# Optimization experiments

Hardware: AMD Instinct MI355X
Metric: run time of the kernel (lower is better)

The kernel has to match this reference:

```python
import jax, jax.numpy as jnp
import numpy as np

B, D, F, H = 256, 9, 8, 256   # batch of trees, tree depth, input features, hidden
N = 2 ** (D + 1) - 1          # total nodes per full binary tree (heap layout)


def _init(key, shape, fan_in):
    return jax.random.normal(key, shape, jnp.float32) * (1.0 / np.sqrt(fan_in))


def setup_inputs() -> dict:
    key = jax.random.key(0)
    ks = jax.random.split(key, 6)
    return {
        "data": jax.random.normal(ks[0], (B, N, F), jnp.float32),
        "Wu": _init(ks[1], (H, F), F),
        "bu": jnp.zeros((H,), jnp.float32),
        "Wr": _init(ks[2], (3 * H, 3 * H), 3 * H),
        "br": jnp.zeros((3 * H,), jnp.float32),
        "Wh": _init(ks[3], (H, 3 * H), 3 * H),
        "bh": jnp.zeros((H,), jnp.float32),
        "Wz": _init(ks[4], (4 * H, 4 * H), 4 * H),
        "bz": jnp.zeros((4 * H,), jnp.float32),
        "Wp": _init(ks[5], (1, H), H),
        "bp": jnp.zeros((1,), jnp.float32),
    }


def reference(data, Wu, bu, Wr, br, Wh, bh, Wz, bz, Wp, bp):
    # data: [B, N, F] node features in heap (level-order) layout;
    # children of the i-th node of level l are nodes 2i, 2i+1 of level l+1.
    b, n_nodes, _ = data.shape
    L = (n_nodes + 1) // 2          # number of leaves
    depth = L.bit_length() - 1
    h_dim = Wu.shape[0]

    # leaf embedding u for every node (leaf() is applied at every tree node)
    u = jnp.einsum('bnf,hf->bnh', data, Wu) + bu          # [B, N, H]
    h = u[:, L - 1:, :]                                    # leaf level states [B, L, H]

    for l in range(depth - 1, -1, -1):                     # bottom-up over levels
        n = 2 ** l
        parent = u[:, n - 1:2 * n - 1, :]                  # [B, n, H]
        h_l, h_r = h[:, 0::2, :], h[:, 1::2, :]            # [B, n, H] each
        hhu = jnp.concatenate([parent, h_l, h_r], axis=-1)  # [B, n, 3H]
        r = jax.nn.sigmoid(jnp.einsum('bnk,jk->bnj', hhu, Wr) + br)
        h_new = jax.nn.relu(jnp.einsum('bnk,hk->bnh', r * hhu, Wh) + bh)
        hhhu = jnp.concatenate([h_new, hhu], axis=-1)      # [B, n, 4H]
        zlin = jnp.einsum('bnk,jk->bnj', hhhu, Wz) + bz    # [B, n, 4H]
        z = jax.nn.softmax(zlin.reshape(b, n, 4, h_dim), axis=2)
        h = (z * hhhu.reshape(b, n, 4, h_dim)).sum(axis=2)  # gated combine -> [B, n, H]

    # h is [B, 1, H] at the root; logits head
    logits = jnp.einsum('bnh,oh->bno', h, Wp) + bp          # [B, 1, 1]
    return logits[:, 0, 0]                                  # [B]
```

## Files before the change

### kernel.cpp

```cpp
#include <hip/hip_runtime.h>
#include <math.h>

#define BB 256
#define NN 1023
#define FF 8
#define HH 256
#define DEPTH 9

enum { EPI_NONE = 0, EPI_SIGMUL = 1, EPI_RELU = 2, EPI_COMBINE = 3 };

typedef __bf16 bf16x8_t __attribute__((ext_vector_type(8)));
typedef float f32x4_t __attribute__((ext_vector_type(4)));

__device__ __forceinline__ void stage16(const void* g, void* l) {
    __builtin_amdgcn_global_load_lds(
        (const __attribute__((address_space(1))) void*)g,
        (__attribute__((address_space(3))) void*)l,
        16, 0, 0);
}

template <int EPI>
__global__ __launch_bounds__(512, 2) void gemm256p(
    const __bf16* __restrict__ A, int lda,
    const __bf16* __restrict__ W,
    const float* __restrict__ bias,
    const __bf16* __restrict__ aux, int ldaux,
    void* __restrict__ Cout, int ldc,
    int K)
{
    __shared__ __bf16 lds[2][2][256 * 64];
    const int tid = threadIdx.x;
    const int lane = tid & 63;
    const int w = tid >> 6;
    const int wr = w >> 2, wc = w & 3;

    const int nwg = gridDim.x * gridDim.y;
    const int hw = blockIdx.y * gridDim.x + blockIdx.x;
    const int xcd = hw & 7, k0 = hw >> 3;
    const int qq = nwg >> 3, rr = nwg & 7;
    const int wg = (xcd < rr ? xcd * (qq + 1) : rr * (qq + 1) + (xcd - rr) * qq) + k0;
    const int bm0 = (wg / gridDim.x) * 256;
    const int bn0 = (wg % gridDim.x) * 256;

    const int srow = tid >> 3;
    const int scolz = ((tid & 7) ^ ((tid >> 3) & 7)) * 8;

    f32x4_t acc[8][4];
#pragma unroll
    for (int i = 0; i < 8; ++i)
#pragma unroll
        for (int j = 0; j < 4; ++j) acc[i][j] = (f32x4_t){0.f, 0.f, 0.f, 0.f};

    const int rA = lane & 15;
    const int klane = (lane >> 4) * 8;
    const int rxor = (lane & 7) * 8;
    const int NT = K >> 6;

#define STAGE_T(t, buf)                                                        \
    do {                                                                       \
        const int kk_ = (t) << 6;                                              \
        _Pragma("unroll")                                                      \
        for (int rnd = 0; rnd < 4; ++rnd) {                                    \
            stage16(A + (size_t)(bm0 + rnd * 64 + srow) * lda + kk_ + scolz,   \
                    &lds[buf][0][rnd * 4096 + w * 512]);                       \
            stage16(W + (size_t)(bn0 + rnd * 64 + srow) * K + kk_ + scolz,     \
                    &lds[buf][1][rnd * 4096 + w * 512]);                       \
        }                                                                      \
    } while (0)

#define LDA_F(As_, i, ks) \
    (*(const bf16x8_t*)&(As_)[(wr * 128 + (i) * 16 + rA) * 64 + (((ks) * 32 + klane) ^ rxor)])
#define LDB_F(Bs_, j, ks) \
    (*(const bf16x8_t*)&(Bs_)[(wc * 64 + (j) * 16 + rA) * 64 + (((ks) * 32 + klane) ^ rxor)])

    STAGE_T(0, 0);
    STAGE_T(1, 1);
    asm volatile("s_waitcnt vmcnt(8)" ::: "memory");
    __builtin_amdgcn_sched_barrier(0);
    __builtin_amdgcn_s_barrier();
    __builtin_amdgcn_sched_barrier(0);

    for (int t = 0; t < NT; ++t) {
        const int p = t & 1;
        const __bf16* As = lds[p][0];
        const __bf16* Bs = lds[p][1];

        bf16x8_t b0[4], b1[4], alo[4], ahi[4];
#pragma unroll
        for (int j = 0; j < 4; ++j) b0[j] = LDB_F(Bs, j, 0);
#pragma unroll
        for (int i = 0; i < 4; ++i) alo[i] = LDA_F(As, i, 0);
#pragma unroll
        for (int i = 0; i < 4; ++i)
#pragma unroll
            for (int j = 0; j < 4; ++j)
                acc[i][j] = __builtin_amdgcn_mfma_f32_16x16x32_bf16(
                    alo[i], b0[j], acc[i][j], 0, 0, 0);
#pragma unroll
        for (int i = 0; i < 4; ++i) ahi[i] = LDA_F(As, 4 + i, 0);
#pragma unroll
        for (int i = 0; i < 4; ++i)
#pragma unroll
            for (int j = 0; j < 4; ++j)
                acc[4 + i][j] = __builtin_amdgcn_mfma_f32_16x16x32_bf16(
                    ahi[i], b0[j], acc[4 + i][j], 0, 0, 0);
#pragma unroll
        for (int j = 0; j < 4; ++j) b1[j] = LDB_F(Bs, j, 1);
#pragma unroll
        for (int i = 0; i < 4; ++i) alo[i] = LDA_F(As, i, 1);
#pragma unroll
        for (int i = 0; i < 4; ++i) ahi[i] = LDA_F(As, 4 + i, 1);
#pragma unroll
        for (int i = 0; i < 4; ++i)
#pragma unroll
            for (int j = 0; j < 4; ++j)
                acc[i][j] = __builtin_amdgcn_mfma_f32_16x16x32_bf16(
                    alo[i], b1[j], acc[i][j], 0, 0, 0);

        asm volatile("s_waitcnt lgkmcnt(0)" ::: "memory");
        __builtin_amdgcn_sched_barrier(0);
        __builtin_amdgcn_s_barrier();
        __builtin_amdgcn_sched_barrier(0);

        if (t + 2 < NT) STAGE_T(t + 2, p);

        __builtin_amdgcn_s_setprio(1);
#pragma unroll
        for (int i = 0; i < 4; ++i)
#pragma unroll
            for (int j = 0; j < 4; ++j)
                acc[4 + i][j] = __builtin_amdgcn_mfma_f32_16x16x32_bf16(
                    ahi[i], b1[j], acc[4 + i][j], 0, 0, 0);
        __builtin_amdgcn_s_setprio(0);

        if (t + 1 < NT) {
            if (t + 2 < NT) {
                asm volatile("s_waitcnt vmcnt(8)" ::: "memory");
            } else {
                asm volatile("s_waitcnt vmcnt(0)" ::: "memory");
            }
            __builtin_amdgcn_sched_barrier(0);
            __builtin_amdgcn_s_barrier();
            __builtin_amdgcn_sched_barrier(0);
        }
    }
#undef STAGE_T
#undef LDA_F
#undef LDB_F

    if (EPI == EPI_COMBINE) {
        const int r = lane & 15;
        const int G = ((bn0 + wc * 64) >> 2) + r;
        float bz4[4];
#pragma unroll
        for (int g = 0; g < 4; ++g) bz4[g] = bias[bn0 + wc * 64 + g * 16 + r];
#pragma unroll
        for (int i = 0; i < 8; ++i) {
#pragma unroll
            for (int reg = 0; reg < 4; ++reg) {
                const int gr = bm0 + wr * 128 + i * 16 + (lane >> 4) * 4 + reg;
                float z0 = acc[i][0][reg] + bz4[0];
                float z1 = acc[i][1][reg] + bz4[1];
                float z2 = acc[i][2][reg] + bz4[2];
                float z3 = acc[i][3][reg] + bz4[3];
                float mx = fmaxf(fmaxf(z0, z1), fmaxf(z2, z3));
                float e0 = __expf(z0 - mx), e1 = __expf(z1 - mx);
                float e2 = __expf(z2 - mx), e3 = __expf(z3 - mx);
                const __bf16* hrow = aux + (size_t)gr * ldaux + G;
                float hv = (e0 * (float)hrow[0] + e1 * (float)hrow[256] +
                            e2 * (float)hrow[512] + e3 * (float)hrow[768]) /
                           (e0 + e1 + e2 + e3);
                ((__bf16*)Cout)[(size_t)gr * ldc + G] = (__bf16)hv;
            }
        }
    } else {
#pragma unroll
        for (int j = 0; j < 4; ++j) {
            const int gc = bn0 + wc * 64 + j * 16 + (lane & 15);
            const float bv = bias[gc];
#pragma unroll
            for (int i = 0; i < 8; ++i) {
#pragma unroll
                for (int reg = 0; reg < 4; ++reg) {
                    const int gr = bm0 + wr * 128 + i * 16 + (lane >> 4) * 4 + reg;
                    float v = acc[i][j][reg] + bv;
                    if (EPI == EPI_SIGMUL) {
                        float s = 1.0f / (1.0f + __expf(-v));
                        v = s * (float)aux[(size_t)gr * ldaux + gc];
                        ((__bf16*)Cout)[(size_t)gr * ldc + gc] = (__bf16)v;
                    } else if (EPI == EPI_RELU) {
                        v = fmaxf(v, 0.0f);
                        ((__bf16*)Cout)[(size_t)gr * ldc + gc] = (__bf16)v;
                    } else {
                        ((float*)Cout)[(size_t)gr * ldc + gc] = v;
                    }
                }
            }
        }
    }
}

template <int EPI>
__global__ __launch_bounds__(256) void gemm_mfma(
    const __bf16* __restrict__ A, int lda,
    const __bf16* __restrict__ W,
    const float* __restrict__ bias,
    const __bf16* __restrict__ aux, int ldaux,
    void* __restrict__ Cout, int ldc,
    int K)
{
    __shared__ __bf16 As[128 * 32];
    __shared__ __bf16 Bs[128 * 32];
    const int tid = threadIdx.x;
    const int lane = tid & 63;
    const int w = tid >> 6;
    const int wr = w >> 1, wc = w & 1;

    const int nwg = gridDim.x * gridDim.y;
    const int hw = blockIdx.y * gridDim.x + blockIdx.x;
    const int xcd = hw & 7, k0 = hw >> 3;
    const int qq = nwg >> 3, rr = nwg & 7;
    const int wg = (xcd < rr ? xcd * (qq + 1) : rr * (qq + 1) + (xcd - rr) * qq) + k0;
    const int bm0 = (wg / gridDim.x) * 128;
    const int bn0 = (wg % gridDim.x) * 128;

    const int srow = lane >> 2;
    const int scol = (lane & 3) * 8;

    f32x4_t acc[4][4];
#pragma unroll
    for (int i = 0; i < 4; ++i)
#pragma unroll
        for (int j = 0; j < 4; ++j) acc[i][j] = (f32x4_t){0.f, 0.f, 0.f, 0.f};

    const int rA = lane & 15;
    const int kslot = (lane >> 4) * 8;

    for (int kk = 0; kk < K; kk += 32) {
        stage16(A + (size_t)(bm0 + w * 16 + srow) * lda + kk + scol,
                &As[(w * 16) * 32]);
        stage16(A + (size_t)(bm0 + 64 + w * 16 + srow) * lda + kk + scol,
                &As[(64 + w * 16) * 32]);
        stage16(W + (size_t)(bn0 + w * 16 + srow) * K + kk + scol,
                &Bs[(w * 16) * 32]);
        stage16(W + (size_t)(bn0 + 64 + w * 16 + srow) * K + kk + scol,
                &Bs[(64 + w * 16) * 32]);
        __syncthreads();

        bf16x8_t af[4], bfr[4];
#pragma unroll
        for (int i = 0; i < 4; ++i)
            af[i] = *(const bf16x8_t*)&As[(wr * 64 + i * 16 + rA) * 32 + kslot];
#pragma unroll
        for (int j = 0; j < 4; ++j)
            bfr[j] = *(const bf16x8_t*)&Bs[(wc * 64 + j * 16 + rA) * 32 + kslot];
#pragma unroll
        for (int i = 0; i < 4; ++i)
#pragma unroll
            for (int j = 0; j < 4; ++j)
                acc[i][j] = __builtin_amdgcn_mfma_f32_16x16x32_bf16(
                    af[i], bfr[j], acc[i][j], 0, 0, 0);
        __syncthreads();
    }

    if (EPI == EPI_COMBINE) {
        const int r = lane & 15;
        const int G = ((bn0 + wc * 64) >> 2) + r;
        float bz4[4];
#pragma unroll
        for (int g = 0; g < 4; ++g) bz4[g] = bias[bn0 + wc * 64 + g * 16 + r];
#pragma unroll
        for (int i = 0; i < 4; ++i) {
#pragma unroll
            for (int reg = 0; reg < 4; ++reg) {
                const int gr = bm0 + wr * 64 + i * 16 + (lane >> 4) * 4 + reg;
                float z0 = acc[i][0][reg] + bz4[0];
                float z1 = acc[i][1][reg] + bz4[1];
                float z2 = acc[i][2][reg] + bz4[2];
                float z3 = acc[i][3][reg] + bz4[3];
                float mx = fmaxf(fmaxf(z0, z1), fmaxf(z2, z3));
                float e0 = __expf(z0 - mx), e1 = __expf(z1 - mx);
                float e2 = __expf(z2 - mx), e3 = __expf(z3 - mx);
                const __bf16* hrow = aux + (size_t)gr * ldaux + G;
                float hv = (e0 * (float)hrow[0] + e1 * (float)hrow[256] +
                            e2 * (float)hrow[512] + e3 * (float)hrow[768]) /
                           (e0 + e1 + e2 + e3);
                ((__bf16*)Cout)[(size_t)gr * ldc + G] = (__bf16)hv;
            }
        }
    } else {
#pragma unroll
        for (int j = 0; j < 4; ++j) {
            const int gc = bn0 + wc * 64 + j * 16 + (lane & 15);
            const float bv = bias[gc];
#pragma unroll
            for (int i = 0; i < 4; ++i) {
#pragma unroll
                for (int reg = 0; reg < 4; ++reg) {
                    const int gr = bm0 + wr * 64 + i * 16 + (lane >> 4) * 4 + reg;
                    float v = acc[i][j][reg] + bv;
                    if (EPI == EPI_SIGMUL) {
                        float s = 1.0f / (1.0f + __expf(-v));
                        v = s * (float)aux[(size_t)gr * ldaux + gc];
                        ((__bf16*)Cout)[(size_t)gr * ldc + gc] = (__bf16)v;
                    } else if (EPI == EPI_RELU) {
                        v = fmaxf(v, 0.0f);
                        ((__bf16*)Cout)[(size_t)gr * ldc + gc] = (__bf16)v;
                    } else {
                        ((float*)Cout)[(size_t)gr * ldc + gc] = v;
                    }
                }
            }
        }
    }
}

__global__ __launch_bounds__(256) void convert_weights(
    const float* __restrict__ Wr, const float* __restrict__ Wh,
    const float* __restrict__ Wz, const float* __restrict__ bz,
    __bf16* __restrict__ Wrb, __bf16* __restrict__ Whb,
    __bf16* __restrict__ Wzb, float* __restrict__ bzp)
{
    const int NR = 768 * 768, NH2 = 256 * 768, NZ = 1024 * 1024;
    const int idx0 = blockIdx.x * 256 + threadIdx.x;
    for (int i = idx0; i < NR + NH2 + NZ; i += gridDim.x * 256) {
        if (i < NR) Wrb[i] = (__bf16)Wr[i];
        else if (i < NR + NH2) Whb[i - NR] = (__bf16)Wh[i - NR];
        else {
            const int z = i - NR - NH2;
            const int p = z >> 10, k = z & 1023;
            const int o = ((p >> 4) & 3) * 256 + (p >> 6) * 16 + (p & 15);
            Wzb[z] = (__bf16)Wz[(size_t)o * 1024 + k];
        }
    }
    if (idx0 < 1024) {
        const int p = idx0;
        const int o = ((p >> 4) & 3) * 256 + (p >> 6) * 16 + (p & 15);
        bzp[p] = bz[o];
    }
}

__global__ __launch_bounds__(256) void build_hhu(
    const float* __restrict__ data, const float* __restrict__ Wu,
    const float* __restrict__ bu, const __bf16* __restrict__ hprev,
    __bf16* __restrict__ hhhu, int l, int r0)
{
    const int n = 1 << l;
    const int row = blockIdx.x * 8 + (threadIdx.x >> 5);
    const int c0 = (threadIdx.x & 31) * 8;
    const int i = r0 + row;
    const int b = i >> l;
    const int m = i & (n - 1);

    float wv[8][8];
#pragma unroll
    for (int cc = 0; cc < 8; ++cc) {
        float4 w0 = *(const float4*)&Wu[(c0 + cc) * 8];
        float4 w1 = *(const float4*)&Wu[(c0 + cc) * 8 + 4];
        wv[cc][0] = w0.x; wv[cc][1] = w0.y; wv[cc][2] = w0.z; wv[cc][3] = w0.w;
        wv[cc][4] = w1.x; wv[cc][5] = w1.y; wv[cc][6] = w1.z; wv[cc][7] = w1.w;
    }
    float buv[8];
#pragma unroll
    for (int cc = 0; cc < 8; ++cc) buv[cc] = bu[c0 + cc];

    __bf16* rowp = hhhu + (size_t)row * 1024;

    {
        const float* dp = data + ((size_t)b * NN + (n - 1) + m) * FF;
        float4 d0 = *(const float4*)dp, d1 = *(const float4*)(dp + 4);
        float dv[8] = {d0.x, d0.y, d0.z, d0.w, d1.x, d1.y, d1.z, d1.w};
        bf16x8_t o;
#pragma unroll
        for (int cc = 0; cc < 8; ++cc) {
            float acc = buv[cc];
#pragma unroll
            for (int f = 0; f < 8; ++f) acc += dv[f] * wv[cc][f];
            o[cc] = (__bf16)acc;
        }
        *(bf16x8_t*)&rowp[256 + c0] = o;
    }

    if (l == 8) {
        const float* dl = data + ((size_t)b * NN + 511 + 2 * m) * FF;
#pragma unroll
        for (int side = 0; side < 2; ++side) {
            const float* dp = dl + side * FF;
            float4 d0 = *(const float4*)dp, d1 = *(const float4*)(dp + 4);
            float dv[8] = {d0.x, d0.y, d0.z, d0.w, d1.x, d1.y, d1.z, d1.w};
            bf16x8_t o;
#pragma unroll
            for (int cc = 0; cc < 8; ++cc) {
                float acc = buv[cc];
#pragma unroll
                for (int f = 0; f < 8; ++f) acc += dv[f] * wv[cc][f];
                o[cc] = (__bf16)acc;
            }
            *(bf16x8_t*)&rowp[512 + side * 256 + c0] = o;
        }
    } else {
        *(bf16x8_t*)&rowp[512 + c0] =
            *(const bf16x8_t*)&hprev[((size_t)b * (2 * n) + 2 * m) * HH + c0];
        *(bf16x8_t*)&rowp[768 + c0] =
            *(const bf16x8_t*)&hprev[((size_t)b * (2 * n) + 2 * m + 1) * HH + c0];
    }
}

__global__ __launch_bounds__(256) void final_kernel(
    const __bf16* __restrict__ hfin, const float* __restrict__ Wp,
    const float* __restrict__ bp, float* __restrict__ out)
{
    const int b = blockIdx.x;
    const int t = threadIdx.x;
    __shared__ float red[256];
    red[t] = (float)hfin[(size_t)b * HH + t] * Wp[t];
    __syncthreads();
    for (int s = 128; s > 0; s >>= 1) {
        if (t < s) red[t] += red[t + s];
        __syncthreads();
    }
    if (t == 0) out[b] = red[0] + bp[0];
}

extern "C" void kernel_launch(void* const* d_in, const int* in_sizes, int n_in,
                              void* d_out, int out_size, void* d_ws, size_t ws_size,
                              hipStream_t stream)
{
    const float* data = (const float*)d_in[0];
    const float* Wu = (const float*)d_in[1];
    const float* bu = (const float*)d_in[2];
    const float* Wr = (const float*)d_in[3];
    const float* br = (const float*)d_in[4];
    const float* Wh = (const float*)d_in[5];
    const float* bh = (const float*)d_in[6];
    const float* Wz = (const float*)d_in[7];
    const float* bz = (const float*)d_in[8];
    const float* Wp = (const float*)d_in[9];
    const float* bp = (const float*)d_in[10];
    float* out = (float*)d_out;

    const size_t CAP = 32768;
    char* w = (char*)d_ws;
    __bf16* hA = (__bf16*)w;   w += (size_t)65536 * HH * 2;
    __bf16* hB = (__bf16*)w;   w += (size_t)32768 * HH * 2;
    __bf16* hhhu = (__bf16*)w; w += CAP * 1024 * 2;
    __bf16* rh = (__bf16*)w;   w += CAP * 768 * 2;
    __bf16* Wrb = (__bf16*)w;  w += (size_t)768 * 768 * 2;
    __bf16* Whb = (__bf16*)w;  w += (size_t)256 * 768 * 2;
    __bf16* Wzb = (__bf16*)w;  w += (size_t)1024 * 1024 * 2;
    float* bzp = (float*)w;    w += 1024 * 4;

    convert_weights<<<2048, 256, 0, stream>>>(Wr, Wh, Wz, bz, Wrb, Whb, Wzb, bzp);

    for (int l = DEPTH - 1; l >= 0; --l) {
        const size_t M = (size_t)BB << l;
        __bf16* dst = ((DEPTH - 1 - l) & 1) ? hB : hA;
        const __bf16* src = ((DEPTH - 1 - l) & 1) ? hA : hB;
        for (size_t r0 = 0; r0 < M; r0 += CAP) {
            const int R = (int)((M - r0 < CAP) ? (M - r0) : CAP);
            build_hhu<<<R / 8, 256, 0, stream>>>(data, Wu, bu, src, hhhu, l, (int)r0);
            if (R >= 2048) {
                gemm256p<EPI_SIGMUL><<<dim3(3, R / 256), 512, 0, stream>>>(
                    hhhu + 256, 1024, Wrb, br, hhhu + 256, 1024, rh, 768, 768);
            } else {
                gemm_mfma<EPI_SIGMUL><<<dim3(6, R / 128), 256, 0, stream>>>(
                    hhhu + 256, 1024, Wrb, br, hhhu + 256, 1024, rh, 768, 768);
            }
            gemm_mfma<EPI_RELU><<<dim3(2, R / 128), 256, 0, stream>>>(
                rh, 768, Whb, bh, nullptr, 0, hhhu, 1024, 768);
            if (R >= 2048) {
                gemm256p<EPI_COMBINE><<<dim3(4, R / 256), 512, 0, stream>>>(
                    hhhu, 1024, Wzb, bzp, hhhu, 1024,
                    dst + (size_t)r0 * HH, HH, 1024);
            } else {
                gemm_mfma<EPI_COMBINE><<<dim3(8, R / 128), 256, 0, stream>>>(
                    hhhu, 1024, Wzb, bzp, hhhu, 1024,
                    dst + (size_t)r0 * HH, HH, 1024);
            }
        }
    }
    final_kernel<<<BB, 256, 0, stream>>>(hA, Wp, bp, out);
}
```

Baseline: 1.240 ms.

## Split GEMM main loop into four phases with interleaved quarter-tile prefetch

The 256x256 bf16 GEMM main loop is reorganised into four barrier-delimited MFMA phases per K-tile. Each phase issues one quarter of the next tile's global-to-LDS loads, A row-quarters and B column-halves, instead of staging whole tiles two iterations ahead. Finer vmcnt waits let a phase start once the part of the tile it needs has landed, and setprio is raised around each MFMA block. Launch bounds drop to one workgroup per CU, trading occupancy for register headroom, and the extra barriers could add synchronisation cost.

```diff
diff --git a/kernel.cpp b/kernel.cpp
--- a/kernel.cpp
+++ b/kernel.cpp
@@ -20,7 +20,7 @@
 }
 
 template <int EPI>
-__global__ __launch_bounds__(512, 2) void gemm256p(
+__global__ __launch_bounds__(512, 1) void gemm256p(
     const __bf16* __restrict__ A, int lda,
     const __bf16* __restrict__ W,
     const float* __restrict__ bias,
@@ -43,7 +43,7 @@
     const int bn0 = (wg % gridDim.x) * 256;
 
     const int srow = tid >> 3;
-    const int scolz = ((tid & 7) ^ ((tid >> 3) & 7)) * 8;
+    const int scolz = ((tid & 7) ^ (srow & 7)) * 8;
 
     f32x4_t acc[8][4];
 #pragma unroll
@@ -56,16 +56,21 @@
     const int rxor = (lane & 7) * 8;
     const int NT = K >> 6;
 
-#define STAGE_T(t, buf)                                                        \
+#define STAGE_A_Q(t, buf, q)                                                   \
     do {                                                                       \
         const int kk_ = (t) << 6;                                              \
-        _Pragma("unroll")                                                      \
-        for (int rnd = 0; rnd < 4; ++rnd) {                                    \
-            stage16(A + (size_t)(bm0 + rnd * 64 + srow) * lda + kk_ + scolz,   \
-                    &lds[buf][0][rnd * 4096 + w * 512]);                       \
-            stage16(W + (size_t)(bn0 + rnd * 64 + srow) * K + kk_ + scolz,     \
-                    &lds[buf][1][rnd * 4096 + w * 512]);                       \
-        }                                                                      \
+        stage16(A + (size_t)(bm0 + (q) * 64 + srow) * lda + kk_ + scolz,       \
+                &lds[buf][0][((q) * 64) * 64 + w * 512]);                      \
+        stage16(A + (size_t)(bm0 + 128 + (q) * 64 + srow) * lda + kk_ + scolz, \
+                &lds[buf][0][((128 + (q) * 64)) * 64 + w * 512]);              \
+    } while (0)
+#define STAGE_B_H(t, buf, hf)                                                  \
+    do {                                                                       \
+        const int kk_ = (t) << 6;                                              \
+        stage16(W + (size_t)(bn0 + (hf) * 128 + srow) * K + kk_ + scolz,       \
+                &lds[buf][1][((hf) * 128) * 64 + w * 512]);                    \
+        stage16(W + (size_t)(bn0 + (hf) * 128 + 64 + srow) * K + kk_ + scolz,  \
+                &lds[buf][1][((hf) * 128 + 64) * 64 + w * 512]);               \
     } while (0)
 
 #define LDA_F(As_, i, ks) \
@@ -73,80 +78,106 @@
 #define LDB_F(Bs_, j, ks) \
     (*(const bf16x8_t*)&(Bs_)[(wc * 64 + (j) * 16 + rA) * 64 + (((ks) * 32 + klane) ^ rxor)])
 
-    STAGE_T(0, 0);
-    STAGE_T(1, 1);
-    asm volatile("s_waitcnt vmcnt(8)" ::: "memory");
+#define PHASE_OPEN()                         \
+    __builtin_amdgcn_sched_barrier(0);       \
+    __builtin_amdgcn_s_barrier();            \
+    asm volatile("s_waitcnt lgkmcnt(0)" ::: "memory"); \
+    __builtin_amdgcn_sched_barrier(0);       \
+    __builtin_amdgcn_s_setprio(1)
+#define PHASE_CLOSE()                        \
+    __builtin_amdgcn_s_setprio(0);           \
+    __builtin_amdgcn_sched_barrier(0);       \
+    __builtin_amdgcn_s_barrier();            \
+    __builtin_amdgcn_sched_barrier(0)
+
+    STAGE_A_Q(0, 0, 0);
+    STAGE_A_Q(0, 0, 1);
+    STAGE_B_H(0, 0, 0);
+    STAGE_B_H(0, 0, 1);
+    asm volatile("s_waitcnt vmcnt(0)" ::: "memory");
     __builtin_amdgcn_sched_barrier(0);
     __builtin_amdgcn_s_barrier();
     __builtin_amdgcn_sched_barrier(0);
 
     for (int t = 0; t < NT; ++t) {
-        const int p = t & 1;
-        const __bf16* As = lds[p][0];
-        const __bf16* Bs = lds[p][1];
-
-        bf16x8_t b0[4], b1[4], alo[4], ahi[4];
+        const int c = t & 1, n = c ^ 1;
+        const __bf16* As = lds[c][0];
+        const __bf16* Bs = lds[c][1];
+        const bool more = (t + 1 < NT);
+        bf16x8_t a0[4], a1[4], b0[4], b1[4];
+
 #pragma unroll
         for (int j = 0; j < 4; ++j) b0[j] = LDB_F(Bs, j, 0);
 #pragma unroll
-        for (int i = 0; i < 4; ++i) alo[i] = LDA_F(As, i, 0);
+        for (int i = 0; i < 4; ++i) a0[i] = LDA_F(As, i, 0);
+        if (more) STAGE_A_Q(t + 1, n, 0);
+        PHASE_OPEN();
 #pragma unroll
         for (int i = 0; i < 4; ++i)
 #pragma unroll
             for (int j = 0; j < 4; ++j)
                 acc[i][j] = __builtin_amdgcn_mfma_f32_16x16x32_bf16(
-                    alo[i], b0[j], acc[i][j], 0, 0, 0);
-#pragma unroll
-        for (int i = 0; i < 4; ++i) ahi[i] = LDA_F(As, 4 + i, 0);
-#pragma unroll
-        for (int i = 0; i < 4; ++i)
-#pragma unroll
-            for (int j = 0; j < 4; ++j)
-                acc[4 + i][j] = __builtin_amdgcn_mfma_f32_16x16x32_bf16(
-                    ahi[i], b0[j], acc[4 + i][j], 0, 0, 0);
+                    a0[i], b0[j], acc[i][j], 0, 0, 0);
+        PHASE_CLOSE();
+
 #pragma unroll
         for (int j = 0; j < 4; ++j) b1[j] = LDB_F(Bs, j, 1);
 #pragma unroll
-        for (int i = 0; i < 4; ++i) alo[i] = LDA_F(As, i, 1);
-#pragma unroll
-        for (int i = 0; i < 4; ++i) ahi[i] = LDA_F(As, 4 + i, 1);
+        for (int i = 0; i < 4; ++i) a1[i] = LDA_F(As, i, 1);
+        if (more) STAGE_B_H(t + 1, n, 0);
+        PHASE_OPEN();
 #pragma unroll
         for (int i = 0; i < 4; ++i)
 #pragma unroll
             for (int j = 0; j < 4; ++j)
                 acc[i][j] = __builtin_amdgcn_mfma_f32_16x16x32_bf16(
-                    alo[i], b1[j], acc[i][j], 0, 0, 0);
-
-        asm volatile("s_waitcnt lgkmcnt(0)" ::: "memory");
+                    a1[i], b1[j], acc[i][j], 0, 0, 0);
+        __builtin_amdgcn_s_setprio(0);
+        if (more) {
+            asm volatile("s_waitcnt vmcnt(4)" ::: "memory");
+        } else {
+            asm volatile("s_waitcnt vmcnt(0)" ::: "memory");
+        }
         __builtin_amdgcn_sched_barrier(0);
         __builtin_amdgcn_s_barrier();
         __builtin_amdgcn_sched_barrier(0);
 
-        if (t + 2 < NT) STAGE_T(t + 2, p);
-
-        __builtin_amdgcn_s_setprio(1);
+#pragma unroll
+        for (int i = 0; i < 4; ++i) a0[i] = LDA_F(As, 4 + i, 0);
+        if (more) STAGE_B_H(t + 1, n, 1);
+        PHASE_OPEN();
 #pragma unroll
         for (int i = 0; i < 4; ++i)
 #pragma unroll
             for (int j = 0; j < 4; ++j)
                 acc[4 + i][j] = __builtin_amdgcn_mfma_f32_16x16x32_bf16(
-                    ahi[i], b1[j], acc[4 + i][j], 0, 0, 0);
+                    a0[i], b0[j], acc[4 + i][j], 0, 0, 0);
+        PHASE_CLOSE();
+
+#pragma unroll
+        for (int i = 0; i < 4; ++i) a1[i] = LDA_F(As, 4 + i, 1);
+        if (more) STAGE_A_Q(t + 1, n, 1);
+        PHASE_OPEN();
+#pragma unroll
+        for (int i = 0; i < 4; ++i)
+#pragma unroll
+            for (int j = 0; j < 4; ++j)
+                acc[4 + i][j] = __builtin_amdgcn_mfma_f32_16x16x32_bf16(
+                    a1[i], b1[j], acc[4 + i][j], 0, 0, 0);
         __builtin_amdgcn_s_setprio(0);
-
-        if (t + 1 < NT) {
-            if (t + 2 < NT) {
-                asm volatile("s_waitcnt vmcnt(8)" ::: "memory");
-            } else {
-                asm volatile("s_waitcnt vmcnt(0)" ::: "memory");
-            }
-            __builtin_amdgcn_sched_barrier(0);
-            __builtin_amdgcn_s_barrier();
-            __builtin_amdgcn_sched_barrier(0);
-        }
-    }
-#undef STAGE_T
+        if (more) {
+            asm volatile("s_waitcnt vmcnt(2)" ::: "memory");
+        }
+        __builtin_amdgcn_sched_barrier(0);
+        __builtin_amdgcn_s_barrier();
+        __builtin_amdgcn_sched_barrier(0);
+    }
+#undef STAGE_A_Q
+#undef STAGE_B_H
 #undef LDA_F
 #undef LDB_F
+#undef PHASE_OPEN
+#undef PHASE_CLOSE
 
     if (EPI == EPI_COMBINE) {
         const int r = lane & 15;
```

After: 1.259 ms. No clear change (+1.5%).

## Use 16-wave workgroups in 256x256 GEMM and XCD-remap build_hhu blocks

Applied to the files above, without the earlier changes.

The 256x256-tile GEMM now launches 1024 threads (16 waves in a 4x4 layout), so each wave owns a 64x64 output subtile instead of 128x64. This halves per-wave accumulators and fragment registers, and each thread stages four 16-byte chunks per k-step instead of eight. The aim is more waves in flight to hide LDS and global latency. It also drops the sched_barrier fences, which gives the compiler more freedom but weakens control of the interleaving. build_hhu block indices are remapped per XCD for locality.

```diff
diff --git a/kernel.cpp b/kernel.cpp
--- a/kernel.cpp
+++ b/kernel.cpp
@@ -19,8 +19,14 @@
         16, 0, 0);
 }
 
+__device__ __forceinline__ int xcd_remap(int hw, int nwg) {
+    const int xcd = hw & 7, k0 = hw >> 3;
+    const int qq = nwg >> 3, rr = nwg & 7;
+    return (xcd < rr ? xcd * (qq + 1) : rr * (qq + 1) + (xcd - rr) * qq) + k0;
+}
+
 template <int EPI>
-__global__ __launch_bounds__(512, 2) void gemm256p(
+__global__ __launch_bounds__(1024, 4) void gemm256w(
     const __bf16* __restrict__ A, int lda,
     const __bf16* __restrict__ W,
     const float* __restrict__ bias,
@@ -36,18 +42,16 @@
 
     const int nwg = gridDim.x * gridDim.y;
     const int hw = blockIdx.y * gridDim.x + blockIdx.x;
-    const int xcd = hw & 7, k0 = hw >> 3;
-    const int qq = nwg >> 3, rr = nwg & 7;
-    const int wg = (xcd < rr ? xcd * (qq + 1) : rr * (qq + 1) + (xcd - rr) * qq) + k0;
+    const int wg = xcd_remap(hw, nwg);
     const int bm0 = (wg / gridDim.x) * 256;
     const int bn0 = (wg % gridDim.x) * 256;
 
     const int srow = tid >> 3;
-    const int scolz = ((tid & 7) ^ ((tid >> 3) & 7)) * 8;
-
-    f32x4_t acc[8][4];
-#pragma unroll
-    for (int i = 0; i < 8; ++i)
+    const int scolz = ((tid & 7) ^ (srow & 7)) * 8;
+
+    f32x4_t acc[4][4];
+#pragma unroll
+    for (int i = 0; i < 4; ++i)
 #pragma unroll
         for (int j = 0; j < 4; ++j) acc[i][j] = (f32x4_t){0.f, 0.f, 0.f, 0.f};
 
@@ -59,106 +63,91 @@
 #define STAGE_T(t, buf)                                                        \
     do {                                                                       \
         const int kk_ = (t) << 6;                                              \
-        _Pragma("unroll")                                                      \
-        for (int rnd = 0; rnd < 4; ++rnd) {                                    \
-            stage16(A + (size_t)(bm0 + rnd * 64 + srow) * lda + kk_ + scolz,   \
-                    &lds[buf][0][rnd * 4096 + w * 512]);                       \
-            stage16(W + (size_t)(bn0 + rnd * 64 + srow) * K + kk_ + scolz,     \
-                    &lds[buf][1][rnd * 4096 + w * 512]);                       \
-        }                                                                      \
+        stage16(A + (size_t)(bm0 + srow) * lda + kk_ + scolz,                  \
+                &lds[buf][0][w * 512]);                                        \
+        stage16(A + (size_t)(bm0 + 128 + srow) * lda + kk_ + scolz,            \
+                &lds[buf][0][8192 + w * 512]);                                 \
+        stage16(W + (size_t)(bn0 + srow) * K + kk_ + scolz,                    \
+                &lds[buf][1][w * 512]);                                        \
+        stage16(W + (size_t)(bn0 + 128 + srow) * K + kk_ + scolz,              \
+                &lds[buf][1][8192 + w * 512]);                                 \
     } while (0)
-
 #define LDA_F(As_, i, ks) \
-    (*(const bf16x8_t*)&(As_)[(wr * 128 + (i) * 16 + rA) * 64 + (((ks) * 32 + klane) ^ rxor)])
+    (*(const bf16x8_t*)&(As_)[(wr * 64 + (i) * 16 + rA) * 64 + (((ks) * 32 + klane) ^ rxor)])
 #define LDB_F(Bs_, j, ks) \
     (*(const bf16x8_t*)&(Bs_)[(wc * 64 + (j) * 16 + rA) * 64 + (((ks) * 32 + klane) ^ rxor)])
 
     STAGE_T(0, 0);
     STAGE_T(1, 1);
-    asm volatile("s_waitcnt vmcnt(8)" ::: "memory");
-    __builtin_amdgcn_sched_barrier(0);
+    asm volatile("s_waitcnt vmcnt(4)" ::: "memory");
     __builtin_amdgcn_s_barrier();
-    __builtin_amdgcn_sched_barrier(0);
 
     for (int t = 0; t < NT; ++t) {
-        const int p = t & 1;
-        const __bf16* As = lds[p][0];
-        const __bf16* Bs = lds[p][1];
-
-        bf16x8_t b0[4], b1[4], alo[4], ahi[4];
-#pragma unroll
-        for (int j = 0; j < 4; ++j) b0[j] = LDB_F(Bs, j, 0);
-#pragma unroll
-        for (int i = 0; i < 4; ++i) alo[i] = LDA_F(As, i, 0);
+        const int cur = t & 1;
+        const __bf16* As = lds[cur][0];
+        const __bf16* Bs = lds[cur][1];
+        bf16x8_t af[4], bf[4];
+
+#pragma unroll
+        for (int j = 0; j < 4; ++j) bf[j] = LDB_F(Bs, j, 0);
+#pragma unroll
+        for (int i = 0; i < 4; ++i) af[i] = LDA_F(As, i, 0);
 #pragma unroll
         for (int i = 0; i < 4; ++i)
 #pragma unroll
             for (int j = 0; j < 4; ++j)
                 acc[i][j] = __builtin_amdgcn_mfma_f32_16x16x32_bf16(
-                    alo[i], b0[j], acc[i][j], 0, 0, 0);
-#pragma unroll
-        for (int i = 0; i < 4; ++i) ahi[i] = LDA_F(As, 4 + i, 0);
-#pragma unroll
-        for (int i = 0; i < 4; ++i)
-#pragma unroll
-            for (int j = 0; j < 4; ++j)
-                acc[4 + i][j] = __builtin_amdgcn_mfma_f32_16x16x32_bf16(
-                    ahi[i], b0[j], acc[4 + i][j], 0, 0, 0);
-#pragma unroll
-        for (int j = 0; j < 4; ++j) b1[j] = LDB_F(Bs, j, 1);
-#pragma unroll
-        for (int i = 0; i < 4; ++i) alo[i] = LDA_F(As, i, 1);
-#pragma unroll
-        for (int i = 0; i < 4; ++i) ahi[i] = LDA_F(As, 4 + i, 1);
-#pragma unroll
-        for (int i = 0; i < 4; ++i)
+                    af[i], bf[j], acc[i][j], 0, 0, 0);
+#pragma unroll
+        for (int j = 0; j < 4; ++j) bf[j] = LDB_F(Bs, j, 1);
+#pragma unroll
+        for (int i = 0; i < 4; ++i) af[i] = LDA_F(As, i, 1);
+#pragma unroll
+        for (int i = 0; i < 2; ++i)
 #pragma unroll
             for (int j = 0; j < 4; ++j)
                 acc[i][j] = __builtin_amdgcn_mfma_f32_16x16x32_bf16(
-                    alo[i], b1[j], acc[i][j], 0, 0, 0);
+                    af[i], bf[j], acc[i][j], 0, 0, 0);
 
         asm volatile("s_waitcnt lgkmcnt(0)" ::: "memory");
-        __builtin_amdgcn_sched_barrier(0);
         __builtin_amdgcn_s_barrier();
-        __builtin_amdgcn_sched_barrier(0);
-
-        if (t + 2 < NT) STAGE_T(t + 2, p);
+        if (t + 2 < NT) STAGE_T(t + 2, cur);
 
         __builtin_amdgcn_s_setprio(1);
 #pragma unroll
-        for (int i = 0; i < 4; ++i)
+        for (int i = 2; i < 4; ++i)
 #pragma unroll
             for (int j = 0; j < 4; ++j)
-                acc[4 + i][j] = __builtin_amdgcn_mfma_f32_16x16x32_bf16(
-                    ahi[i], b1[j], acc[4 + i][j], 0, 0, 0);
+                acc[i][j] = __builtin_amdgcn_mfma_f32_16x16x32_bf16(
+                    af[i], bf[j], acc[i][j], 0, 0, 0);
         __builtin_amdgcn_s_setprio(0);
 
         if (t + 1 < NT) {
             if (t + 2 < NT) {
-                asm volatile("s_waitcnt vmcnt(8)" ::: "memory");
+                asm volatile("s_waitcnt vmcnt(4)" ::: "memory");
             } else {
                 asm volatile("s_waitcnt vmcnt(0)" ::: "memory");
             }
-            __builtin_amdgcn_sched_barrier(0);
             __builtin_amdgcn_s_barrier();
-            __builtin_amdgcn_sched_barrier(0);
         }
     }
 #undef STAGE_T
 #undef LDA_F
 #undef LDB_F
 
+    const int hi = lane >> 4;
+    const int r = lane & 15;
+
     if (EPI == EPI_COMBINE) {
-        const int r = lane & 15;
         const int G = ((bn0 + wc * 64) >> 2) + r;
         float bz4[4];
 #pragma unroll
         for (int g = 0; g < 4; ++g) bz4[g] = bias[bn0 + wc * 64 + g * 16 + r];
 #pragma unroll
-        for (int i = 0; i < 8; ++i) {
+        for (int i = 0; i < 4; ++i) {
 #pragma unroll
             for (int reg = 0; reg < 4; ++reg) {
-                const int gr = bm0 + wr * 128 + i * 16 + (lane >> 4) * 4 + reg;
+                const int gr = bm0 + wr * 64 + i * 16 + hi * 4 + reg;
                 float z0 = acc[i][0][reg] + bz4[0];
                 float z1 = acc[i][1][reg] + bz4[1];
                 float z2 = acc[i][2][reg] + bz4[2];
@@ -176,13 +165,13 @@
     } else {
 #pragma unroll
         for (int j = 0; j < 4; ++j) {
-            const int gc = bn0 + wc * 64 + j * 16 + (lane & 15);
+            const int gc = bn0 + wc * 64 + j * 16 + r;
             const float bv = bias[gc];
 #pragma unroll
-            for (int i = 0; i < 8; ++i) {
+            for (int i = 0; i < 4; ++i) {
 #pragma unroll
                 for (int reg = 0; reg < 4; ++reg) {
-                    const int gr = bm0 + wr * 128 + i * 16 + (lane >> 4) * 4 + reg;
+                    const int gr = bm0 + wr * 64 + i * 16 + hi * 4 + reg;
                     float v = acc[i][j][reg] + bv;
                     if (EPI == EPI_SIGMUL) {
                         float s = 1.0f / (1.0f + __expf(-v));
@@ -218,9 +207,7 @@
 
     const int nwg = gridDim.x * gridDim.y;
     const int hw = blockIdx.y * gridDim.x + blockIdx.x;
-    const int xcd = hw & 7, k0 = hw >> 3;
-    const int qq = nwg >> 3, rr = nwg & 7;
-    const int wg = (xcd < rr ? xcd * (qq + 1) : rr * (qq + 1) + (xcd - rr) * qq) + k0;
+    const int wg = xcd_remap(hw, nwg);
     const int bm0 = (wg / gridDim.x) * 128;
     const int bn0 = (wg % gridDim.x) * 128;
 
@@ -346,7 +333,8 @@
     __bf16* __restrict__ hhhu, int l, int r0)
 {
     const int n = 1 << l;
-    const int row = blockIdx.x * 8 + (threadIdx.x >> 5);
+    const int blk = xcd_remap(blockIdx.x, gridDim.x);
+    const int row = blk * 8 + (threadIdx.x >> 5);
     const int c0 = (threadIdx.x & 31) * 8;
     const int i = r0 + row;
     const int b = i >> l;
@@ -460,7 +448,7 @@
             const int R = (int)((M - r0 < CAP) ? (M - r0) : CAP);
             build_hhu<<<R / 8, 256, 0, stream>>>(data, Wu, bu, src, hhhu, l, (int)r0);
             if (R >= 2048) {
-                gemm256p<EPI_SIGMUL><<<dim3(3, R / 256), 512, 0, stream>>>(
+                gemm256w<EPI_SIGMUL><<<dim3(3, R / 256), 1024, 0, stream>>>(
                     hhhu + 256, 1024, Wrb, br, hhhu + 256, 1024, rh, 768, 768);
             } else {
                 gemm_mfma<EPI_SIGMUL><<<dim3(6, R / 128), 256, 0, stream>>>(
@@ -469,7 +457,7 @@
             gemm_mfma<EPI_RELU><<<dim3(2, R / 128), 256, 0, stream>>>(
                 rh, 768, Whb, bh, nullptr, 0, hhhu, 1024, 768);
             if (R >= 2048) {
-                gemm256p<EPI_COMBINE><<<dim3(4, R / 256), 512, 0, stream>>>(
+                gemm256w<EPI_COMBINE><<<dim3(4, R / 256), 1024, 0, stream>>>(
                     hhhu, 1024, Wzb, bzp, hhhu, 1024,
                     dst + (size_t)r0 * HH, HH, 1024);
             } else {
```

Result: no change. 1.228 ms (-0.9%).
